# Kernel optimization log

Hardware: AMD Instinct MI355X
Metric: run time of the kernel (lower is better)

The kernel has to match this reference:

```python
import jax, jax.numpy as jnp
import numpy as np

N = 100000      # num nodes
E = 800000      # num edges
IN = 256        # in_features
D = 64          # out_features per head
H = 4           # num_heads
EF = 64         # edge_feats
NET = 8         # num_etype
SLOPE = 0.2     # leaky relu negative slope


def setup_inputs() -> dict:
    key = jax.random.key(0)
    ks = jax.random.split(key, 12)
    s = 0.05
    h = jax.random.normal(ks[0], (N, IN), jnp.float32)
    row = jax.random.randint(ks[1], (E,), 0, N, dtype=jnp.int32)   # src
    col = jax.random.randint(ks[2], (E,), 0, N, dtype=jnp.int32)   # dst
    tp = jax.random.randint(ks[3], (E,), 0, NET, dtype=jnp.int32)  # edge type
    W = jax.random.normal(ks[4], (IN, D * H), jnp.float32) * s
    W_e = jax.random.normal(ks[5], (EF, EF * H), jnp.float32) * s
    edge_emb = jax.random.normal(ks[6], (NET, EF), jnp.float32) * s
    a_l = jax.random.normal(ks[7], (1, H, D), jnp.float32) * s
    a_r = jax.random.normal(ks[8], (1, H, D), jnp.float32) * s
    a_e = jax.random.normal(ks[9], (1, H, EF), jnp.float32) * s
    res_W = jax.random.normal(ks[10], (IN, D * H), jnp.float32) * s
    res_b = jnp.zeros((D * H,), jnp.float32)
    return {"h": h, "W": W, "W_e": W_e, "edge_emb": edge_emb,
            "a_l": a_l, "a_r": a_r, "a_e": a_e,
            "res_W": res_W, "res_b": res_b,
            "row": row, "col": col, "tp": tp}


def reference(h, W, W_e, edge_emb, a_l, a_r, a_e, res_W, res_b, row, col, tp):
    # node projection -> [N, H, D]; nan-guard as in the original
    emb = jnp.nan_to_num((h @ W).reshape(-1, H, D), nan=0.0)
    # edge-type embedding projection -> [NET, H, EF]
    e = (edge_emb @ W_e).reshape(-1, H, EF)
    # per-edge attention logits [E, H]
    h_l = (a_l * emb).sum(-1)[row]
    h_r = (a_r * emb).sum(-1)[col]
    h_e = (a_e * e).sum(-1)[tp]
    att = jax.nn.leaky_relu(h_l + h_r + h_e, SLOPE)
    # segment softmax over edges grouped by destination node
    m = jax.ops.segment_max(att, col, num_segments=N)          # [N, H]
    ex = jnp.exp(att - m[col])                                 # [E, H]
    denom = jax.ops.segment_sum(ex, col, num_segments=N)      # [N, H]
    alpha = ex / denom[col]                                    # [E, H]
    # gather-multiply-scatter message passing: [E, H, D] -> [N, H, D]
    msg = emb[row] * alpha[:, :, None]
    out = jax.ops.segment_sum(msg, col, num_segments=N).reshape(N, H * D)
    # residual linear + elu activation
    out = out + h @ res_W + res_b
    return jax.nn.elu(out)
```

## Files before the change

### kernel.cpp

```cpp
#include <hip/hip_runtime.h>

#define N_NODES 100000
#define E_EDGES 800000
#define IN_F 256
#define D_HEAD 64
#define H_HEADS 4
#define EF_F 64
#define NET_T 8
#define HD 256
#define SLOPE 0.2f
#define NTILES ((N_NODES + 63) / 64)
#define NGROUP ((NTILES + 7) / 8)
#define EPT 8
#define HBLOCKS ((E_EDGES + 256 * EPT - 1) / (256 * EPT))

typedef unsigned short u16;
typedef unsigned long long u64;
typedef __attribute__((ext_vector_type(8))) short bf16x8;
typedef __attribute__((ext_vector_type(4))) float f32x4;

static __device__ __forceinline__ u16 f2bf(float f) {
    unsigned int u = __float_as_uint(f);
    unsigned int r = u + 0x7FFFu + ((u >> 16) & 1u);
    return (u16)(r >> 16);
}
static __device__ __forceinline__ float bf2f(unsigned int u) {
    return __uint_as_float(u << 16);
}

__global__ void k_pre(const float* __restrict__ W, const float* __restrict__ resW,
                      u16* __restrict__ Bfrag,
                      const float* __restrict__ edge_emb, const float* __restrict__ W_e,
                      const float* __restrict__ a_e, float* __restrict__ s_e) {
    const int b = blockIdx.x;
    const int tid = threadIdx.x;
    if (b < 64) {
        const int gid = b * 256 + tid;
        const int lane = gid & 63;
        const int fragid = gid >> 6;
        const int n = fragid & 3;
        const int ks = (fragid >> 2) & 7;
        const int g = fragid >> 5;
        const int c = g * 64 + n * 16 + (lane & 15);
        const int k0 = ks * 32 + (lane >> 4) * 8;
        const float* src = (c < HD) ? &W[c] : &resW[c - HD];
        u16 tmp[8];
#pragma unroll
        for (int j = 0; j < 8; ++j)
            tmp[j] = f2bf(src[(size_t)(k0 + j) * HD]);
        *reinterpret_cast<uint4*>(&Bfrag[(size_t)fragid * 512 + lane * 8]) =
            *reinterpret_cast<const uint4*>(tmp);
    } else {
        const int t  = tid >> 5;
        const int h  = (tid >> 3) & 3;
        const int fc = tid & 7;
        float part = 0.f;
        for (int j = 0; j < 8; ++j) {
            const int f = fc * 8 + j;
            float acc = 0.f;
            for (int k = 0; k < EF_F; ++k)
                acc += edge_emb[t * EF_F + k] * W_e[k * (EF_F * H_HEADS) + h * EF_F + f];
            part += a_e[h * EF_F + f] * acc;
        }
        for (int off = 1; off < 8; off <<= 1)
            part += __shfl_xor(part, off, 64);
        if (fc == 0) s_e[t * H_HEADS + h] = part;
    }
}

__global__ void k_hist(const int* __restrict__ col, int* __restrict__ counts) {
    const int base = (blockIdx.x * 256 + threadIdx.x) * EPT;
    if (base + EPT <= E_EDGES) {
        const int4 c0 = *reinterpret_cast<const int4*>(&col[base]);
        const int4 c1 = *reinterpret_cast<const int4*>(&col[base + 4]);
        atomicAdd(&counts[c0.x], 1);
        atomicAdd(&counts[c0.y], 1);
        atomicAdd(&counts[c0.z], 1);
        atomicAdd(&counts[c0.w], 1);
        atomicAdd(&counts[c1.x], 1);
        atomicAdd(&counts[c1.y], 1);
        atomicAdd(&counts[c1.z], 1);
        atomicAdd(&counts[c1.w], 1);
    } else {
        for (int e = base; e < E_EDGES; ++e)
            atomicAdd(&counts[col[e]], 1);
    }
}

__global__ __launch_bounds__(256, 3)
void k_mfma(const float* __restrict__ A, const u16* __restrict__ Bfrag,
            const float* __restrict__ a_l, const float* __restrict__ a_r,
            const float* __restrict__ resb,
            u16* __restrict__ emb_bf, float* __restrict__ s_l, float* __restrict__ s_r,
            u16* __restrict__ res_bf) {
    __shared__ char At[32768];
    const int tid = threadIdx.x;
    const int lane = tid & 63;
    const int wv = tid >> 6;
    const int gidx = blockIdx.x >> 4;
    const int x = blockIdx.x & 15;
    const int tile = gidx * 8 + (x & 7);
    if (tile >= NTILES) return;
    const int by = x >> 3;
    const int wid = (by << 2) | wv;
    const int row0 = tile * 64;

#pragma unroll
    for (int half = 0; half < 2; ++half) {
        float4 v[8];
#pragma unroll
        for (int c = 0; c < 8; ++c) {
            const int lin8 = (half * 8 + c) * 2048 + tid * 8;
            const int r_lin = lin8 >> 9;
            int grow = row0 + r_lin;
            if (grow >= N_NODES) grow = N_NODES - 1;
            const int colb = lin8 & 511;
            v[c] = *reinterpret_cast<const float4*>(&A[(size_t)grow * IN_F + (colb >> 1)]);
        }
#pragma unroll
        for (int c = 0; c < 8; ++c) {
            const int lin8 = (half * 8 + c) * 2048 + tid * 8;
            const int r_lin = lin8 >> 9;
            uint2 o;
            o.x = (unsigned)f2bf(v[c].x) | ((unsigned)f2bf(v[c].y) << 16);
            o.y = (unsigned)f2bf(v[c].z) | ((unsigned)f2bf(v[c].w) << 16);
            *reinterpret_cast<uint2*>(&At[lin8 ^ ((r_lin & 7) << 4)]) = o;
        }
    }
    __syncthreads();

    const int lr = lane & 15;
    const int lg = lane >> 4;
    const int xr = (lr & 7) << 4;
    const int klg = lg * 16;

    int rowbase[4];
#pragma unroll
    for (int m = 0; m < 4; ++m) rowbase[m] = (m * 16 + lr) * 512;

    const u16* bp = Bfrag + (size_t)wid * 16384 + lane * 8;

    f32x4 acc[4][4] = {};
#pragma unroll
    for (int ks = 0; ks < 8; ++ks) {
        bf16x8 af[4], bfr[4];
        const int kx = ((ks << 6) + klg) ^ xr;
#pragma unroll
        for (int n = 0; n < 4; ++n)
            bfr[n] = *reinterpret_cast<const bf16x8*>(&bp[ks * 2048 + n * 512]);
#pragma unroll
        for (int m = 0; m < 4; ++m)
            af[m] = *reinterpret_cast<const bf16x8*>(&At[rowbase[m] + kx]);
#pragma unroll
        for (int m = 0; m < 4; ++m)
#pragma unroll
            for (int n = 0; n < 4; ++n)
                acc[m][n] = __builtin_amdgcn_mfma_f32_16x16x32_bf16(bfr[n], af[m], acc[m][n], 0, 0, 0);
    }

    if (by == 0) {
        const int h = wv;
        float4 alv[4], arv[4];
#pragma unroll
        for (int n = 0; n < 4; ++n) {
            alv[n] = *reinterpret_cast<const float4*>(&a_l[h * D_HEAD + n * 16 + lg * 4]);
            arv[n] = *reinterpret_cast<const float4*>(&a_r[h * D_HEAD + n * 16 + lg * 4]);
        }
#pragma unroll
        for (int m = 0; m < 4; ++m) {
            const int node = row0 + m * 16 + lr;
            float dl = 0.f, dr = 0.f;
            u64 pk[4];
#pragma unroll
            for (int n = 0; n < 4; ++n) {
                float v0 = acc[m][n][0], v1 = acc[m][n][1], v2 = acc[m][n][2], v3 = acc[m][n][3];
                v0 = isnan(v0) ? 0.f : v0;
                v1 = isnan(v1) ? 0.f : v1;
                v2 = isnan(v2) ? 0.f : v2;
                v3 = isnan(v3) ? 0.f : v3;
                dl += v0 * alv[n].x + v1 * alv[n].y + v2 * alv[n].z + v3 * alv[n].w;
                dr += v0 * arv[n].x + v1 * arv[n].y + v2 * arv[n].z + v3 * arv[n].w;
                pk[n] = (u64)f2bf(v0) | ((u64)f2bf(v1) << 16) |
                        ((u64)f2bf(v2) << 32) | ((u64)f2bf(v3) << 48);
            }
            if (node < N_NODES) {
                const size_t base = (size_t)node * HD + h * D_HEAD + lg * 4;
#pragma unroll
                for (int n = 0; n < 4; ++n)
                    *reinterpret_cast<u64*>(&emb_bf[base + n * 16]) = pk[n];
            }
            dl += __shfl_xor(dl, 16, 64); dr += __shfl_xor(dr, 16, 64);
            dl += __shfl_xor(dl, 32, 64); dr += __shfl_xor(dr, 32, 64);
            if (lg == 0 && node < N_NODES) {
                s_l[node * H_HEADS + h] = dl;
                s_r[node * H_HEADS + h] = dr;
            }
        }
    } else {
        const int c0 = wv * 64 + lg * 4;
        float4 rb[4];
#pragma unroll
        for (int n = 0; n < 4; ++n)
            rb[n] = *reinterpret_cast<const float4*>(&resb[c0 + n * 16]);
#pragma unroll
        for (int m = 0; m < 4; ++m) {
            const int node = row0 + m * 16 + lr;
            if (node < N_NODES) {
                const size_t base = (size_t)node * HD + c0;
#pragma unroll
                for (int n = 0; n < 4; ++n) {
                    const float v0 = acc[m][n][0] + rb[n].x;
                    const float v1 = acc[m][n][1] + rb[n].y;
                    const float v2 = acc[m][n][2] + rb[n].z;
                    const float v3 = acc[m][n][3] + rb[n].w;
                    const u64 pk = (u64)f2bf(v0) | ((u64)f2bf(v1) << 16) |
                                   ((u64)f2bf(v2) << 32) | ((u64)f2bf(v3) << 48);
                    *reinterpret_cast<u64*>(&res_bf[base + n * 16]) = pk;
                }
            }
        }
    }
}

__global__ void k_scan1(const int* __restrict__ counts, int* __restrict__ row_ptr,
                        int* __restrict__ partials) {
    __shared__ int sd[256];
    const int t = threadIdx.x, b = blockIdx.x;
    const int base = b * 1024 + t * 4;
    int v[4];
#pragma unroll
    for (int j = 0; j < 4; ++j) v[j] = (base + j < N_NODES) ? counts[base + j] : 0;
    const int s = v[0] + v[1] + v[2] + v[3];
    sd[t] = s;
    __syncthreads();
    for (int off = 1; off < 256; off <<= 1) {
        int y = (t >= off) ? sd[t - off] : 0;
        __syncthreads();
        sd[t] += y;
        __syncthreads();
    }
    int p = sd[t] - s;
#pragma unroll
    for (int j = 0; j < 4; ++j) {
        if (base + j < N_NODES) row_ptr[base + j] = p;
        p += v[j];
    }
    if (t == 255) partials[b] = sd[255];
}

__global__ void k_scan2(int* __restrict__ partials) {
    __shared__ int sd[128];
    const int t = threadIdx.x;
    const int v = (t < 98) ? partials[t] : 0;
    sd[t] = v;
    __syncthreads();
    for (int off = 1; off < 128; off <<= 1) {
        int y = (t >= off) ? sd[t - off] : 0;
        __syncthreads();
        sd[t] += y;
        __syncthreads();
    }
    if (t < 98) partials[t] = sd[t] - v;
}

__global__ void k_scan3(int* __restrict__ row_ptr, int* __restrict__ fill,
                        const int* __restrict__ partials) {
    const int i = blockIdx.x * 256 + threadIdx.x;
    if (i < N_NODES) {
        const int v = row_ptr[i] + partials[i >> 10];
        row_ptr[i] = v;
        fill[i] = v;
    }
    if (i == 0) row_ptr[N_NODES] = E_EDGES;
}

__global__ void k_scatter(const int* __restrict__ row, const int* __restrict__ col,
                          const int* __restrict__ tp, const float* __restrict__ s_l,
                          const float* __restrict__ s_r, const float* __restrict__ s_e,
                          int* __restrict__ fill, int* __restrict__ perm_row,
                          float4* __restrict__ exw_perm) {
    const int e = blockIdx.x * 256 + threadIdx.x;
    if (e >= E_EDGES) return;
    const int r = row[e], c = col[e], t = tp[e];
    const float4 sl = *reinterpret_cast<const float4*>(&s_l[r * 4]);
    const float4 sr = *reinterpret_cast<const float4*>(&s_r[c * 4]);
    const float4 se = *reinterpret_cast<const float4*>(&s_e[t * 4]);
    float4 ex;
    float x;
    x = sl.x + sr.x + se.x; x = (x > 0.f) ? x : SLOPE * x; ex.x = __expf(x);
    x = sl.y + sr.y + se.y; x = (x > 0.f) ? x : SLOPE * x; ex.y = __expf(x);
    x = sl.z + sr.z + se.z; x = (x > 0.f) ? x : SLOPE * x; ex.z = __expf(x);
    x = sl.w + sr.w + se.w; x = (x > 0.f) ? x : SLOPE * x; ex.w = __expf(x);
    const int p = atomicAdd(&fill[c], 1);
    perm_row[p] = r;
    exw_perm[p] = ex;
}

__global__ __launch_bounds__(256)
void k_aggregate(const int* __restrict__ row_ptr, const int* __restrict__ perm_row,
                 const float* __restrict__ exw_perm,
                 const u16* __restrict__ emb_bf, const u16* __restrict__ res_bf,
                 float* __restrict__ outp) {
    const int wave = threadIdx.x >> 6;
    const int lane = threadIdx.x & 63;
    const int n = blockIdx.x * 4 + wave;
    const int h = lane >> 4;
    const int start = row_ptr[n], end = row_ptr[n + 1];
    const size_t o = (size_t)n * HD + lane * 4;
    const u64 rv = *reinterpret_cast<const u64*>(&res_bf[o]);

    float a0 = 0.f, a1 = 0.f, a2 = 0.f, a3 = 0.f, den = 0.f;
    for (int i = start; i < end; i += 8) {
        int r[8]; float ex[8]; u64 ev[8];
#pragma unroll
        for (int j = 0; j < 8; ++j) {
            const int idx = (i + j < end) ? (i + j) : (end - 1);
            r[j] = perm_row[idx];
        }
#pragma unroll
        for (int j = 0; j < 8; ++j) {
            const int idx = (i + j < end) ? (i + j) : (end - 1);
            ex[j] = (i + j < end) ? exw_perm[idx * 4 + h] : 0.f;
        }
#pragma unroll
        for (int j = 0; j < 8; ++j)
            ev[j] = *reinterpret_cast<const u64*>(&emb_bf[(size_t)r[j] * HD + lane * 4]);
#pragma unroll
        for (int j = 0; j < 8; ++j) {
            const unsigned lo = (unsigned)ev[j], hi = (unsigned)(ev[j] >> 32);
            a0 += ex[j] * __uint_as_float(lo << 16);
            a1 += ex[j] * __uint_as_float(lo & 0xFFFF0000u);
            a2 += ex[j] * __uint_as_float(hi << 16);
            a3 += ex[j] * __uint_as_float(hi & 0xFFFF0000u);
            den += ex[j];
        }
    }
    const float inv = (den > 0.f) ? 1.f / den : 0.f;
    f32x4 out;
    float x;
    x = a0 * inv + bf2f((unsigned)(rv) & 0xFFFFu);       out.x = (x > 0.f) ? x : __expf(x) - 1.f;
    x = a1 * inv + bf2f((unsigned)(rv >> 16) & 0xFFFFu); out.y = (x > 0.f) ? x : __expf(x) - 1.f;
    x = a2 * inv + bf2f((unsigned)(rv >> 32) & 0xFFFFu); out.z = (x > 0.f) ? x : __expf(x) - 1.f;
    x = a3 * inv + bf2f((unsigned)(rv >> 48) & 0xFFFFu); out.w = (x > 0.f) ? x : __expf(x) - 1.f;
    __builtin_nontemporal_store(out, reinterpret_cast<f32x4*>(&outp[o]));
}

extern "C" void kernel_launch(void* const* d_in, const int* in_sizes, int n_in,
                              void* d_out, int out_size, void* d_ws, size_t ws_size,
                              hipStream_t stream) {
    const float* h    = (const float*)d_in[0];
    const float* W    = (const float*)d_in[1];
    const float* W_e  = (const float*)d_in[2];
    const float* eemb = (const float*)d_in[3];
    const float* a_l  = (const float*)d_in[4];
    const float* a_r  = (const float*)d_in[5];
    const float* a_e  = (const float*)d_in[6];
    const float* resW = (const float*)d_in[7];
    const float* resb = (const float*)d_in[8];
    const int* row = (const int*)d_in[9];
    const int* col = (const int*)d_in[10];
    const int* tp  = (const int*)d_in[11];
    float* outp = (float*)d_out;

    char* ws = (char*)d_ws;
    size_t off = 0;
    auto alloc = [&](size_t b) { size_t o = off; off += (b + 255) & ~(size_t)255; return o; };
    u16*  Bfrag   = (u16*)(ws + alloc((size_t)512 * IN_F * 2));
    u16*  emb_bf  = (u16*)(ws + alloc((size_t)N_NODES * HD * 2));
    u16*  res_bf  = (u16*)(ws + alloc((size_t)N_NODES * HD * 2));
    float* s_l    = (float*)(ws + alloc((size_t)N_NODES * H_HEADS * 4));
    float* s_r    = (float*)(ws + alloc((size_t)N_NODES * H_HEADS * 4));
    float* s_e    = (float*)(ws + alloc(NET_T * H_HEADS * 4));
    int*  counts  = (int*)(ws + alloc((size_t)N_NODES * 4));
    int*  row_ptr = (int*)(ws + alloc((size_t)(N_NODES + 1) * 4));
    int*  fill    = (int*)(ws + alloc((size_t)N_NODES * 4));
    int*  perm_row= (int*)(ws + alloc((size_t)E_EDGES * 4));
    float* exw_perm=(float*)(ws + alloc((size_t)E_EDGES * H_HEADS * 4));
    int*  partials= (int*)(ws + alloc(128 * 4));

    (void)hipMemsetAsync(counts, 0, (size_t)N_NODES * 4, stream);
    k_pre<<<65, 256, 0, stream>>>(W, resW, Bfrag, eemb, W_e, a_e, s_e);
    k_hist<<<HBLOCKS, 256, 0, stream>>>(col, counts);
    k_mfma<<<NGROUP * 16, 256, 0, stream>>>(h, Bfrag, a_l, a_r, resb, emb_bf, s_l, s_r, res_bf);
    k_scan1<<<98, 256, 0, stream>>>(counts, row_ptr, partials);
    k_scan2<<<1, 128, 0, stream>>>(partials);
    k_scan3<<<(N_NODES + 255) / 256, 256, 0, stream>>>(row_ptr, fill, partials);
    k_scatter<<<(E_EDGES + 255) / 256, 256, 0, stream>>>(row, col, tp, s_l, s_r, s_e,
                                                         fill, perm_row, (float4*)exw_perm);
    k_aggregate<<<N_NODES / 4, 256, 0, stream>>>(row_ptr, perm_row, exw_perm, emb_bf, res_bf, outp);
}
```

Measured before the change: 286.3 us.

## Move attention logit computation into aggregate and pack row/type into one index

The scatter pass no longer computes per-edge exp weights or writes a 16-byte-per-edge float4 array. It only writes a packed int (row | type<<20), and each thread now handles 8 edges using vectorized loads. The aggregate kernel recomputes the leaky-relu and exp logits from s_l (gathered by row), s_r (per destination node) and s_e. This removes roughly 16 MB of write plus read traffic, at the cost of an extra gathered s_l load and an exp per edge in the aggregation loop.

```diff
diff --git a/kernel.cpp b/kernel.cpp
--- a/kernel.cpp
+++ b/kernel.cpp
@@ -275,30 +275,45 @@
 }
 
 __global__ void k_scatter(const int* __restrict__ row, const int* __restrict__ col,
-                          const int* __restrict__ tp, const float* __restrict__ s_l,
-                          const float* __restrict__ s_r, const float* __restrict__ s_e,
-                          int* __restrict__ fill, int* __restrict__ perm_row,
-                          float4* __restrict__ exw_perm) {
-    const int e = blockIdx.x * 256 + threadIdx.x;
-    if (e >= E_EDGES) return;
-    const int r = row[e], c = col[e], t = tp[e];
-    const float4 sl = *reinterpret_cast<const float4*>(&s_l[r * 4]);
-    const float4 sr = *reinterpret_cast<const float4*>(&s_r[c * 4]);
-    const float4 se = *reinterpret_cast<const float4*>(&s_e[t * 4]);
-    float4 ex;
-    float x;
-    x = sl.x + sr.x + se.x; x = (x > 0.f) ? x : SLOPE * x; ex.x = __expf(x);
-    x = sl.y + sr.y + se.y; x = (x > 0.f) ? x : SLOPE * x; ex.y = __expf(x);
-    x = sl.z + sr.z + se.z; x = (x > 0.f) ? x : SLOPE * x; ex.z = __expf(x);
-    x = sl.w + sr.w + se.w; x = (x > 0.f) ? x : SLOPE * x; ex.w = __expf(x);
-    const int p = atomicAdd(&fill[c], 1);
-    perm_row[p] = r;
-    exw_perm[p] = ex;
+                          const int* __restrict__ tp, int* __restrict__ fill,
+                          int* __restrict__ perm_rt) {
+    const int base = (blockIdx.x * 256 + threadIdx.x) * EPT;
+    if (base + EPT <= E_EDGES) {
+        const int4 r0 = *reinterpret_cast<const int4*>(&row[base]);
+        const int4 r1 = *reinterpret_cast<const int4*>(&row[base + 4]);
+        const int4 c0 = *reinterpret_cast<const int4*>(&col[base]);
+        const int4 c1 = *reinterpret_cast<const int4*>(&col[base + 4]);
+        const int4 t0 = *reinterpret_cast<const int4*>(&tp[base]);
+        const int4 t1 = *reinterpret_cast<const int4*>(&tp[base + 4]);
+        int p[8];
+        p[0] = atomicAdd(&fill[c0.x], 1);
+        p[1] = atomicAdd(&fill[c0.y], 1);
+        p[2] = atomicAdd(&fill[c0.z], 1);
+        p[3] = atomicAdd(&fill[c0.w], 1);
+        p[4] = atomicAdd(&fill[c1.x], 1);
+        p[5] = atomicAdd(&fill[c1.y], 1);
+        p[6] = atomicAdd(&fill[c1.z], 1);
+        p[7] = atomicAdd(&fill[c1.w], 1);
+        perm_rt[p[0]] = r0.x | (t0.x << 20);
+        perm_rt[p[1]] = r0.y | (t0.y << 20);
+        perm_rt[p[2]] = r0.z | (t0.z << 20);
+        perm_rt[p[3]] = r0.w | (t0.w << 20);
+        perm_rt[p[4]] = r1.x | (t1.x << 20);
+        perm_rt[p[5]] = r1.y | (t1.y << 20);
+        perm_rt[p[6]] = r1.z | (t1.z << 20);
+        perm_rt[p[7]] = r1.w | (t1.w << 20);
+    } else {
+        for (int e = base; e < E_EDGES; ++e) {
+            const int p = atomicAdd(&fill[col[e]], 1);
+            perm_rt[p] = row[e] | (tp[e] << 20);
+        }
+    }
 }
 
 __global__ __launch_bounds__(256)
-void k_aggregate(const int* __restrict__ row_ptr, const int* __restrict__ perm_row,
-                 const float* __restrict__ exw_perm,
+void k_aggregate(const int* __restrict__ row_ptr, const int* __restrict__ perm_rt,
+                 const float* __restrict__ s_l, const float* __restrict__ s_r,
+                 const float* __restrict__ s_e,
                  const u16* __restrict__ emb_bf, const u16* __restrict__ res_bf,
                  float* __restrict__ outp) {
     const int wave = threadIdx.x >> 6;
@@ -308,31 +323,36 @@
     const int start = row_ptr[n], end = row_ptr[n + 1];
     const size_t o = (size_t)n * HD + lane * 4;
     const u64 rv = *reinterpret_cast<const u64*>(&res_bf[o]);
+    const float srh = s_r[n * H_HEADS + h];
 
     float a0 = 0.f, a1 = 0.f, a2 = 0.f, a3 = 0.f, den = 0.f;
     for (int i = start; i < end; i += 8) {
-        int r[8]; float ex[8]; u64 ev[8];
+        int r[8], t[8]; float sl[8]; u64 ev[8];
 #pragma unroll
         for (int j = 0; j < 8; ++j) {
             const int idx = (i + j < end) ? (i + j) : (end - 1);
-            r[j] = perm_row[idx];
-        }
-#pragma unroll
-        for (int j = 0; j < 8; ++j) {
-            const int idx = (i + j < end) ? (i + j) : (end - 1);
-            ex[j] = (i + j < end) ? exw_perm[idx * 4 + h] : 0.f;
-        }
+            const int q = perm_rt[idx];
+            r[j] = q & 0xFFFFF;
+            t[j] = q >> 20;
+        }
+#pragma unroll
+        for (int j = 0; j < 8; ++j)
+            sl[j] = s_l[r[j] * H_HEADS + h];
 #pragma unroll
         for (int j = 0; j < 8; ++j)
             ev[j] = *reinterpret_cast<const u64*>(&emb_bf[(size_t)r[j] * HD + lane * 4]);
 #pragma unroll
         for (int j = 0; j < 8; ++j) {
+            float lg = sl[j] + srh + s_e[t[j] * H_HEADS + h];
+            lg = (lg > 0.f) ? lg : SLOPE * lg;
+            float ex = __expf(lg);
+            ex = (i + j < end) ? ex : 0.f;
             const unsigned lo = (unsigned)ev[j], hi = (unsigned)(ev[j] >> 32);
-            a0 += ex[j] * __uint_as_float(lo << 16);
-            a1 += ex[j] * __uint_as_float(lo & 0xFFFF0000u);
-            a2 += ex[j] * __uint_as_float(hi << 16);
-            a3 += ex[j] * __uint_as_float(hi & 0xFFFF0000u);
-            den += ex[j];
+            a0 += ex * __uint_as_float(lo << 16);
+            a1 += ex * __uint_as_float(lo & 0xFFFF0000u);
+            a2 += ex * __uint_as_float(hi << 16);
+            a3 += ex * __uint_as_float(hi & 0xFFFF0000u);
+            den += ex;
         }
     }
     const float inv = (den > 0.f) ? 1.f / den : 0.f;
@@ -374,8 +394,7 @@
     int*  counts  = (int*)(ws + alloc((size_t)N_NODES * 4));
     int*  row_ptr = (int*)(ws + alloc((size_t)(N_NODES + 1) * 4));
     int*  fill    = (int*)(ws + alloc((size_t)N_NODES * 4));
-    int*  perm_row= (int*)(ws + alloc((size_t)E_EDGES * 4));
-    float* exw_perm=(float*)(ws + alloc((size_t)E_EDGES * H_HEADS * 4));
+    int*  perm_rt = (int*)(ws + alloc((size_t)E_EDGES * 4));
     int*  partials= (int*)(ws + alloc(128 * 4));
 
     (void)hipMemsetAsync(counts, 0, (size_t)N_NODES * 4, stream);
@@ -385,7 +404,7 @@
     k_scan1<<<98, 256, 0, stream>>>(counts, row_ptr, partials);
     k_scan2<<<1, 128, 0, stream>>>(partials);
     k_scan3<<<(N_NODES + 255) / 256, 256, 0, stream>>>(row_ptr, fill, partials);
-    k_scatter<<<(E_EDGES + 255) / 256, 256, 0, stream>>>(row, col, tp, s_l, s_r, s_e,
-                                                         fill, perm_row, (float4*)exw_perm);
-    k_aggregate<<<N_NODES / 4, 256, 0, stream>>>(row_ptr, perm_row, exw_perm, emb_bf, res_bf, outp);
-}
+    k_scatter<<<HBLOCKS, 256, 0, stream>>>(row, col, tp, fill, perm_rt);
+    k_aggregate<<<N_NODES / 4, 256, 0, stream>>>(row_ptr, perm_rt, s_l, s_r, s_e,
+                                                 emb_bf, res_bf, outp);
+}
```

Result: no change. 290.2 us (+1.4%).
